# Kernel tuning notes

Hardware: AMD Instinct MI355X
Metric: run time of the kernel (lower is better)

The kernel has to match this reference:

```python
import jax, jax.numpy as jnp
from jax import lax
import numpy as np

NUM_REGIONS = 64
REGION_SIZE = 8
TAU = 13
ETA = 0.8
BINS = 100


def _histc(v, bins=BINS):
    # torch.histc semantics: bins span [min, max]; value==max lands in last bin.
    vmin, vmax = v.min(), v.max()
    idx = jnp.clip(((v - vmin) / (vmax - vmin) * bins), 0, bins - 1).astype(jnp.int32)
    return jnp.bincount(idx, length=bins).astype(jnp.float32)


def setup_inputs() -> dict:
    key = jax.random.key(0)
    x = jax.random.normal(key, (4, 8, 16, 256, 256), dtype=jnp.float32)
    return {"input_tensor": x}


def reference(input_tensor):
    B, T, C, H, W = input_tensor.shape
    rs = REGION_SIZE
    gh, gw = H // rs, W // rs
    G = gh * gw
    nf = T - 1
    R = NUM_REGIONS

    # preprocess: (B,T,C,gh,rs,gw,rs) -> (B,T,C,gh,gw,rs,rs) -> (B,T,C,G,rs,rs)
    fm = input_tensor.reshape(B, T, C, gh, rs, gw, rs)
    fm = fm.transpose(0, 1, 2, 3, 5, 4, 6).reshape(B, T, C, G, rs, rs)

    # motion information (per-batch histogram mutual information)
    motion = fm[:, 1:] - fm[:, :-1]                      # (B,nf,C,G,rs,rs)
    x_t = fm[:, :-1].reshape(B, -1)
    x_t1 = fm[:, 1:].reshape(B, -1)
    n_el = x_t.shape[1]

    h_joint = jax.vmap(_histc)(x_t * x_t1)               # (B,100)
    h_x = jax.vmap(_histc)(x_t) / n_el
    h_x1 = jax.vmap(_histc)(x_t1) / n_el
    p_joint = h_joint / h_joint.sum(-1, keepdims=True)
    p_x = h_x / h_x.sum(-1, keepdims=True)
    p_x1 = h_x1 / h_x1.sum(-1, keepdims=True)
    mi = (p_joint * (jnp.log(p_joint + 1e-10) - jnp.log(p_x * p_x1 + 1e-10))).sum(-1)  # (B,)
    corr = (np.e ** ETA) / jnp.tanh(jnp.log(mi))
    motion = motion + corr[:, None, None, None, None, None]

    # select top regions: sum over channels, topk over G*rs*rs flattened
    mag = motion.reshape(B, nf, C, -1).sum(axis=2)       # (B,nf,G*rs*rs)
    _, top_idx = lax.top_k(mag, R)                       # (B,nf,R)

    # spatial centers (faithful to original: divisor is num_regions)
    y_idx = top_idx // R
    x_idx = top_idx % R
    cy = (y_idx * rs + rs // 2).astype(jnp.float32)
    cx = (x_idx * rs + rs // 2).astype(jnp.float32)
    centers = jnp.stack([cy, cx], axis=-1)               # (B,nf,R,2)

    mean_c = centers.mean(axis=2, keepdims=True)
    d = centers - mean_c
    cov = jnp.einsum('bfri,bfrj->bfij', d, d) / (R - 1)  # (B,nf,2,2)
    inv_cov = jnp.linalg.inv(cov + 1e-6 * jnp.eye(2, dtype=cov.dtype))

    # diff = centers.unsqueeze(2) - centers.unsqueeze(3) -> (B,nf,R,R,2)
    diff = centers[:, :, None, :, :] - centers[:, :, :, None, :]
    v = jnp.einsum('bfqre,bfed->bfqrd', diff, inv_cov)
    maha = jnp.sqrt(v * diff).sum(-1)                    # (B,nf,R,R)

    # graph: mark tau^2 smallest distances with 1
    flat = maha.reshape(B, nf, R * R)
    _, ti = lax.top_k(-flat, TAU * TAU)                  # smallest
    b_ix = jnp.arange(B)[:, None, None]
    f_ix = jnp.arange(nf)[None, :, None]
    graph = jnp.zeros_like(flat).at[b_ix, f_ix, ti].set(1.0)
    return graph.reshape(B, nf, R, R)
```

## Files before the change

kernel.cpp:

```cpp
#include <hip/hip_runtime.h>
#include <stdint.h>


typedef unsigned int u32;
typedef unsigned long long u64;

#define BB 4
#define TT 8
#define CC 16
#define HWN 65536
#define NF 7
#define FRAME 1048576LL
#define NELF 7340032.0f
#define NPAIR 28
#define SEG 65536

#define WS_MM 0
#define WS_CORR 128
#define WS_WCNT 144
#define WS_MAG 16384
#define WS_MMPART (WS_MAG)
#define WS_HISTC  (WS_MAG + 65536)
#define WS_NEED (16384 + 28LL*65536*4)

__device__ __forceinline__ u32 encf(float f) {
  u32 u = __float_as_uint(f);
  return (u & 0x80000000u) ? ~u : (u | 0x80000000u);
}
__device__ __forceinline__ float decf(u32 e) {
  u32 u = (e & 0x80000000u) ? (e ^ 0x80000000u) : ~e;
  return __uint_as_float(u);
}

__global__ void k_minmax_pass(const float* __restrict__ x, u32* __restrict__ part) {
  const int blk = blockIdx.x;
  const int b = blk >> 9;
  const long long w0 = (long long)(blk & 511) * 2048;
  const int tid = threadIdx.x;
  u32 mn0 = 0xFFFFFFFFu, mx0 = 0u, mn1 = 0xFFFFFFFFu, mx1 = 0u,
      mnp = 0xFFFFFFFFu, mxp = 0u;
  float4 pv0, pv1;
  for (int t = 0; t < 8; ++t) {
    const float4* fp = (const float4*)(x + ((long long)(b * TT + t)) * FRAME + w0);
    float4 v0 = fp[tid];
    float4 v1 = fp[tid + 256];
#define MM_COMP(vc, pc)                                                     \
    {                                                                       \
      u32 ev = encf(vc);                                                    \
      if (t < 7) { mn0 = min(mn0, ev); mx0 = max(mx0, ev); }                \
      if (t > 0) {                                                          \
        mn1 = min(mn1, ev); mx1 = max(mx1, ev);                             \
        u32 ep = encf(__fmul_rn(pc, vc));                                   \
        mnp = min(mnp, ep); mxp = max(mxp, ep);                             \
      }                                                                     \
    }
    MM_COMP(v0.x, pv0.x) MM_COMP(v0.y, pv0.y) MM_COMP(v0.z, pv0.z) MM_COMP(v0.w, pv0.w)
    MM_COMP(v1.x, pv1.x) MM_COMP(v1.y, pv1.y) MM_COMP(v1.z, pv1.z) MM_COMP(v1.w, pv1.w)
#undef MM_COMP
    pv0 = v0; pv1 = v1;
  }
  __shared__ u32 sm[6][256];
  sm[0][tid] = mn0; sm[1][tid] = mx0; sm[2][tid] = mn1;
  sm[3][tid] = mx1; sm[4][tid] = mnp; sm[5][tid] = mxp;
  __syncthreads();
  for (int st = 128; st > 0; st >>= 1) {
    if (tid < st) {
      sm[0][tid] = min(sm[0][tid], sm[0][tid + st]);
      sm[1][tid] = max(sm[1][tid], sm[1][tid + st]);
      sm[2][tid] = min(sm[2][tid], sm[2][tid + st]);
      sm[3][tid] = max(sm[3][tid], sm[3][tid + st]);
      sm[4][tid] = min(sm[4][tid], sm[4][tid + st]);
      sm[5][tid] = max(sm[5][tid], sm[5][tid + st]);
    }
    __syncthreads();
  }
  if (tid == 0) {
    u32* o = part + blk * 6;
    o[0] = sm[0][0]; o[1] = sm[1][0]; o[2] = sm[2][0];
    o[3] = sm[3][0]; o[4] = sm[4][0]; o[5] = sm[5][0];
  }
}

__global__ void k_mm_reduce(const u32* __restrict__ part, u32* __restrict__ mm) {
  const int b = blockIdx.x;
  const int tid = threadIdx.x;
  const u32* p0 = part + (b * 512 + tid) * 6;
  const u32* p1 = p0 + 256 * 6;
  __shared__ u32 sm[6][256];
  sm[0][tid] = min(p0[0], p1[0]); sm[1][tid] = max(p0[1], p1[1]);
  sm[2][tid] = min(p0[2], p1[2]); sm[3][tid] = max(p0[3], p1[3]);
  sm[4][tid] = min(p0[4], p1[4]); sm[5][tid] = max(p0[5], p1[5]);
  __syncthreads();
  for (int st = 128; st > 0; st >>= 1) {
    if (tid < st) {
      sm[0][tid] = min(sm[0][tid], sm[0][tid + st]);
      sm[1][tid] = max(sm[1][tid], sm[1][tid + st]);
      sm[2][tid] = min(sm[2][tid], sm[2][tid + st]);
      sm[3][tid] = max(sm[3][tid], sm[3][tid + st]);
      sm[4][tid] = min(sm[4][tid], sm[4][tid + st]);
      sm[5][tid] = max(sm[5][tid], sm[5][tid + st]);
    }
    __syncthreads();
  }
  if (tid == 0)
    for (int i = 0; i < 6; ++i) mm[b * 6 + i] = sm[i][0];
}

__device__ __forceinline__ int bin_of(float v, float vmin, float den) {
  float tt = __fsub_rn(v, vmin);
  float q = __fdiv_rn(tt, den);
  float z = __fmul_rn(q, 100.0f);
  z = fminf(fmaxf(z, 0.0f), 99.0f);
  return (int)z;
}

__global__ void k_hist_pass(const float* __restrict__ x, const u32* __restrict__ mm,
                            u32* __restrict__ histc) {
  __shared__ u32 h[300 * 16];
  for (int i = threadIdx.x; i < 4800; i += 256) h[i] = 0u;
  __syncthreads();
  const int blk = blockIdx.x;
  const int b = blk >> 9;
  const long long w0 = (long long)(blk & 511) * 2048;
  const int tid = threadIdx.x;
  const int sub = tid & 15;
  float mn_t = decf(mm[6 * b + 0]), den_t = __fsub_rn(decf(mm[6 * b + 1]), decf(mm[6 * b + 0]));
  float mn_1 = decf(mm[6 * b + 2]), den_1 = __fsub_rn(decf(mm[6 * b + 3]), decf(mm[6 * b + 2]));
  float mn_p = decf(mm[6 * b + 4]), den_p = __fsub_rn(decf(mm[6 * b + 5]), decf(mm[6 * b + 4]));
  float prev[8];
  for (int t = 0; t < 8; ++t) {
    const float* fp = x + ((long long)(b * TT + t)) * FRAME + w0 + tid;
#pragma unroll
    for (int k = 0; k < 8; ++k) {
      float v = fp[k << 8];
      if (t < 7) atomicAdd(&h[bin_of(v, mn_t, den_t) * 16 + sub], 1u);
      if (t > 0) {
        atomicAdd(&h[(100 + bin_of(v, mn_1, den_1)) * 16 + sub], 1u);
        float p = __fmul_rn(prev[k], v);
        atomicAdd(&h[(200 + bin_of(p, mn_p, den_p)) * 16 + sub], 1u);
      }
      prev[k] = v;
    }
  }
  __syncthreads();
  u32* dst = histc + blk * 300;
  for (int i = threadIdx.x; i < 300; i += 256) {
    u32 s = 0;
#pragma unroll
    for (int c = 0; c < 16; ++c) s += h[i * 16 + c];
    dst[i] = s;
  }
}

__device__ float tanh_emul(float a) {
  const float kClamp = 7.90531110763549805f;
  float xx = fminf(fmaxf(a, -kClamp), kClamp);
  float x2 = __fmul_rn(xx, xx);
  float p = __fmaf_rn(x2, -2.76076847742355e-16f, 2.00018790482477e-13f);
  p = __fmaf_rn(x2, p, -8.60467152213735e-11f);
  p = __fmaf_rn(x2, p, 5.12229709037114e-08f);
  p = __fmaf_rn(x2, p, 1.48572235717979e-05f);
  p = __fmaf_rn(x2, p, 6.37261928875436e-04f);
  p = __fmaf_rn(x2, p, 4.89352455891786e-03f);
  p = __fmul_rn(xx, p);
  float q = __fmaf_rn(x2, 1.19825839466702e-06f, 1.18534705686654e-04f);
  q = __fmaf_rn(x2, q, 2.26843463243900e-03f);
  q = __fmaf_rn(x2, q, 4.89352518554385e-03f);
  float r = __fdiv_rn(p, q);
  if (fabsf(a) < 0.0004f) r = a;
  return r;
}

__global__ void __launch_bounds__(256) k_corr(const u32* __restrict__ histc,
                                              float* __restrict__ corr) {
  const int b = blockIdx.x;
  const int tid = threadIdx.x;
  __shared__ u32 shist[300];
  __shared__ float shx[100], shx1[100], sterm[100];
  __shared__ float ssum[3];
  for (int i = tid; i < 300; i += 256) {
    const u32* src = histc + (long long)(b * 512) * 300 + i;
    u32 s0 = 0, s1 = 0, s2 = 0, s3 = 0, s4 = 0, s5 = 0, s6 = 0, s7 = 0;
    for (int c = 0; c < 512; c += 8) {
      s0 += src[(c + 0) * 300]; s1 += src[(c + 1) * 300];
      s2 += src[(c + 2) * 300]; s3 += src[(c + 3) * 300];
      s4 += src[(c + 4) * 300]; s5 += src[(c + 5) * 300];
      s6 += src[(c + 6) * 300]; s7 += src[(c + 7) * 300];
    }
    shist[i] = ((s0 + s1) + (s2 + s3)) + ((s4 + s5) + (s6 + s7));
  }
  __syncthreads();
  const u32* HX = shist;
  const u32* HX1 = shist + 100;
  const u32* HJ = shist + 200;
  if (tid < 100) {
    shx[tid] = __fdiv_rn((float)HX[tid], NELF);
    shx1[tid] = __fdiv_rn((float)HX1[tid], NELF);
  }
  __syncthreads();
  if (tid == 0) {
    float Sj = 0.0f;
    for (int i = 0; i < 100; ++i) Sj = __fadd_rn(Sj, (float)HJ[i]);
    float Sx = 0.0f, Sx1 = 0.0f;
    for (int i = 0; i < 100; ++i) Sx = __fadd_rn(Sx, shx[i]);
    for (int i = 0; i < 100; ++i) Sx1 = __fadd_rn(Sx1, shx1[i]);
    ssum[0] = Sj; ssum[1] = Sx; ssum[2] = Sx1;
  }
  __syncthreads();
  if (tid < 100) {
    float Sj = ssum[0], Sx = ssum[1], Sx1 = ssum[2];
    float pj = __fdiv_rn((float)HJ[tid], Sj);
    float px = __fdiv_rn(shx[tid], Sx);
    float px1 = __fdiv_rn(shx1[tid], Sx1);
    float la = (float)log((double)__fadd_rn(pj, 1e-10f));
    float lb = (float)log((double)__fadd_rn(__fmul_rn(px, px1), 1e-10f));
    sterm[tid] = __fmul_rn(pj, __fsub_rn(la, lb));
  }
  __syncthreads();
  if (tid == 0) {
    float mi = 0.0f;
    for (int i = 0; i < 100; ++i) mi = __fadd_rn(mi, sterm[i]);
    float lm = (float)log((double)mi);
    float th = tanh_emul(lm);
    float num = (float)exp(0.8);
    corr[b] = __fdiv_rn(num, th);
  }
}

__global__ void k_mag_all(const float* __restrict__ x, const float* __restrict__ corr,
                          float* __restrict__ mag) {
  int gid = blockIdx.x * 256 + threadIdx.x;
  int b = gid >> 16;
  int hw = gid & 65535;
  int row = hw >> 8, col = hw & 255;
  int g = (row >> 3) * 32 + (col >> 3);
  int s = g * 64 + (row & 7) * 8 + (col & 7);
  const float cb = corr[b];
  const float* xp = x + (long long)b * TT * FRAME + hw;
  float acc[7] = {0.f, 0.f, 0.f, 0.f, 0.f, 0.f, 0.f};
  for (int c = 0; c < CC; ++c) {
    float v[8];
#pragma unroll
    for (int t = 0; t < 8; ++t)
      v[t] = xp[(long long)(t * CC + c) << 16];
#pragma unroll
    for (int f = 0; f < 7; ++f)
      acc[f] = __fadd_rn(acc[f], __fadd_rn(__fsub_rn(v[f + 1], v[f]), cb));
  }
#pragma unroll
  for (int f = 0; f < 7; ++f)
    mag[(((long long)(b * NF + f)) << 16) + s] = acc[f];
}

__global__ void __launch_bounds__(64) k_top64_local(const float* __restrict__ mag,
                                                    u64* __restrict__ cand,
                                                    u32* __restrict__ wcnt) {
  const int blk = blockIdx.x;
  const int bf = blk >> 4;
  const int wid = blk & 15;
  const int lane = threadIdx.x;
  const int wbase_elem = wid * 4096;
  const float4* m4 = (const float4*)(mag + (long long)bf * SEG + wbase_elem);

  u32 e[64];
#pragma unroll
  for (int k = 0; k < 16; ++k) {
    float4 v = m4[k * 64 + lane];
    e[4 * k + 0] = encf(v.x); e[4 * k + 1] = encf(v.y);
    e[4 * k + 2] = encf(v.z); e[4 * k + 3] = encf(v.w);
  }
  u32 T = 0u;
  for (int bit = 31; bit >= 0; --bit) {
    u32 Tt = T | (1u << bit);
    u32 c = 0;
#pragma unroll
    for (int k = 0; k < 64; ++k) c += (e[k] >= Tt) ? 1u : 0u;
#pragma unroll
    for (int off = 1; off < 64; off <<= 1) c += __shfl_xor(c, off, 64);
    if (c >= 64u) T = Tt;
  }

  u64* dst = cand + (long long)bf * 2048 + wid * 128;
  u32 run = 0;
  const u64 below = (lane == 0) ? 0ull : (~0ull >> (64 - lane));
#pragma unroll
  for (int k = 0; k < 64; ++k) {
    bool cnd = (e[k] >= T);
    u64 mask = __ballot(cnd);
    if (cnd) {
      u32 off = run + (u32)__popcll(mask & below);
      if (off < 128u) {
        int s = wbase_elem + (k >> 2) * 256 + lane * 4 + (k & 3);
        dst[off] = ((u64)e[k] << 32) | (u64)(0xFFFFFFFFu - (u32)s);
      }
    }
    run += (u32)__popcll(mask);
  }
  if (lane == 0) wcnt[bf * 16 + wid] = (run < 128u) ? run : 128u;
}

__global__ void __launch_bounds__(1024) k_merge_graph(const u64* __restrict__ cand,
                                                      const u32* __restrict__ wcnt,
                                                      float* __restrict__ out) {
  const int bf = blockIdx.x;
  const int tid = threadIdx.x;
  __shared__ u64 candk[2048];
  __shared__ u32 wbase[17];
  __shared__ float cy[64], cx[64];
  __shared__ float sinv[4];
  __shared__ u32 keys[4096];
  __shared__ u32 bins[256 * 16];
  __shared__ u32 stot[256];
  __shared__ u32 tie[4096];
  __shared__ u32 scal[4];

  if (tid == 0) {
    u32 acc = 0;
    for (int w = 0; w < 16; ++w) { wbase[w] = acc; acc += wcnt[bf * 16 + w]; }
    wbase[16] = acc;
  }
  __syncthreads();
  for (int w = 0; w < 16; ++w) {
    u32 cnt = wbase[w + 1] - wbase[w];
    for (u32 s = tid; s < cnt; s += 1024)
      candk[wbase[w] + s] = cand[(long long)bf * 2048 + w * 128 + s];
  }
  __syncthreads();
  u32 n = wbase[16];

  for (u32 i = tid; i < n; i += 1024) {
    u64 mine = candk[i];
    int rank = 0;
    for (u32 j = 0; j < n; ++j) rank += (candk[j] > mine) ? 1 : 0;
    if (rank < 64) {
      int idx = (int)(0xFFFFFFFFu - (u32)(mine & 0xFFFFFFFFull));
      cy[rank] = (float)((idx >> 6) * 8 + 4);
      cx[rank] = (float)((idx & 63) * 8 + 4);
    }
  }
  __syncthreads();

  if (tid == 0) {
    float sy = 0.f, sx = 0.f;
    for (int r = 0; r < 64; ++r) sy = __fadd_rn(sy, cy[r]);
    for (int r = 0; r < 64; ++r) sx = __fadd_rn(sx, cx[r]);
    float my = __fdiv_rn(sy, 64.0f), mx = __fdiv_rn(sx, 64.0f);
    float c00 = 0.f, c01 = 0.f, c11 = 0.f;
    for (int r = 0; r < 64; ++r) {
      float dy = __fsub_rn(cy[r], my);
      float dx = __fsub_rn(cx[r], mx);
      c00 = __fadd_rn(c00, __fmul_rn(dy, dy));
      c01 = __fadd_rn(c01, __fmul_rn(dy, dx));
      c11 = __fadd_rn(c11, __fmul_rn(dx, dx));
    }
    c00 = __fdiv_rn(c00, 63.0f); c01 = __fdiv_rn(c01, 63.0f); c11 = __fdiv_rn(c11, 63.0f);
    c00 = __fadd_rn(c00, 1e-6f); c11 = __fadd_rn(c11, 1e-6f);
    double det = (double)c00 * (double)c11 - (double)c01 * (double)c01;
    sinv[0] = (float)((double)c11 / det);
    sinv[1] = (float)(-(double)c01 / det);
    sinv[2] = sinv[1];
    sinv[3] = (float)((double)c00 / det);
  }
  __syncthreads();

  float i00 = sinv[0], i01 = sinv[1], i10 = sinv[2], i11 = sinv[3];
  long long obase = (long long)bf * 4096;
  for (int ee = tid; ee < 4096; ee += 1024) {
    int q = ee >> 6, r = ee & 63;
    float d0 = __fsub_rn(cy[r], cy[q]);
    float d1 = __fsub_rn(cx[r], cx[q]);
    float v0 = __fadd_rn(__fadd_rn(0.0f, __fmul_rn(d0, i00)), __fmul_rn(d1, i10));
    float v1 = __fadd_rn(__fadd_rn(0.0f, __fmul_rn(d0, i01)), __fmul_rn(d1, i11));
    float p0 = __fmul_rn(v0, d0);
    float p1 = __fmul_rn(v1, d1);
    float s0 = __fsqrt_rn(p0);
    float s1 = __fsqrt_rn(p1);
    float mh = __fadd_rn(__fadd_rn(0.0f, s0), s1);
    u32 key;
    if (mh != mh) key = 0xFFFFFFFFu;
    else key = encf(-mh);
    keys[ee] = key;
    out[obase + ee] = 0.0f;
  }
  __syncthreads();

  u32 prefix = 0u, need = 169u;
  for (int pass = 0; pass < 4; ++pass) {
    int shift = 24 - pass * 8;
    if (tid == 0) scal[2] = 0u;
    for (int i = tid; i < 4096; i += 1024) bins[i] = 0u;
    __syncthreads();
    for (int k = 0; k < 4; ++k) {
      u32 ky = keys[tid + (k << 10)];
      bool ok = (pass == 0) || ((ky >> (shift + 8)) == (prefix >> (shift + 8)));
      if (ok) atomicAdd(&bins[(((ky >> shift) & 0xFFu) << 4) + (tid & 15)], 1u);
    }
    __syncthreads();
    if (tid < 256) {
      u32 s = 0;
#pragma unroll
      for (int c = 0; c < 16; ++c) s += bins[(tid << 4) + c];
      stot[tid] = s;
    }
    __syncthreads();
    for (int off = 1; off < 256; off <<= 1) {
      u32 v = 0;
      if (tid < 256) {
        v = stot[tid];
        if (tid + off < 256) v += stot[tid + off];
      }
      __syncthreads();
      if (tid < 256) stot[tid] = v;
      __syncthreads();
    }
    if (tid < 256) {
      u32 si = stot[tid];
      u32 snext = (tid < 255) ? stot[tid + 1] : 0u;
      if (si >= need && snext < need) {
        scal[0] = prefix | ((u32)tid << shift);
        scal[1] = need - snext;
      }
    }
    __syncthreads();
    prefix = scal[0]; need = scal[1];
    __syncthreads();
  }
  for (int k = 0; k < 4; ++k) {
    int ee = tid + (k << 10);
    u32 ky = keys[ee];
    if (ky > prefix) out[obase + ee] = 1.0f;
    else if (ky == prefix) {
      u32 p = atomicAdd(&scal[2], 1u);
      tie[p] = (u32)ee;
    }
  }
  __syncthreads();
  int tc = (int)scal[2];
  for (int i = tid; i < tc; i += 1024) {
    u32 ei = tie[i];
    int rank = 0;
    for (int j = 0; j < tc; ++j) rank += (tie[j] < ei);
    if (rank < (int)need) out[obase + ei] = 1.0f;
  }
}

extern "C" void kernel_launch(void* const* d_in, const int* in_sizes, int n_in,
                              void* d_out, int out_size, void* d_ws, size_t ws_size,
                              hipStream_t stream) {
  if (ws_size < (size_t)WS_NEED) return;
  const float* x = (const float*)d_in[0];
  float* out = (float*)d_out;
  char* ws = (char*)d_ws;
  u32* mm = (u32*)(ws + WS_MM);
  float* corr = (float*)(ws + WS_CORR);
  u32* wcnt = (u32*)(ws + WS_WCNT);
  float* mag = (float*)(ws + WS_MAG);
  u32* mmpart = (u32*)(ws + WS_MMPART);
  u32* histc = (u32*)(ws + WS_HISTC);
  u64* cand = (u64*)d_out;

  hipLaunchKernelGGL(k_minmax_pass, dim3(2048), dim3(256), 0, stream, x, mmpart);
  hipLaunchKernelGGL(k_mm_reduce, dim3(4), dim3(256), 0, stream, mmpart, mm);
  hipLaunchKernelGGL(k_hist_pass, dim3(2048), dim3(256), 0, stream, x, mm, histc);
  hipLaunchKernelGGL(k_corr, dim3(4), dim3(256), 0, stream, histc, corr);
  hipLaunchKernelGGL(k_mag_all, dim3(1024), dim3(256), 0, stream, x, corr, mag);
  hipLaunchKernelGGL(k_top64_local, dim3(448), dim3(64), 0, stream, mag, cand, wcnt);
  hipLaunchKernelGGL(k_merge_graph, dim3(28), dim3(1024), 0, stream, cand, wcnt, out);
}
```

Baseline: 211.7 us.

## Vectorize hist and mag loads with float4, widen shared histogram privatization

The histogram pass now loads four floats per thread with float4 and uses 32 sub-histograms instead of 16, so the shared-memory atomics contend less. Its reduction reads the copies with a rotated index to avoid bank conflicts. The magnitude kernel processes four pixels per thread with float4 loads and stores, launching a quarter of the blocks. The merge kernel's radix bins are likewise widened to 32 copies, which doubles shared memory use and may reduce occupancy.

```diff
diff --git a/kernel.cpp b/kernel.cpp
--- a/kernel.cpp
+++ b/kernel.cpp
@@ -116,38 +116,43 @@
 
 __global__ void k_hist_pass(const float* __restrict__ x, const u32* __restrict__ mm,
                             u32* __restrict__ histc) {
-  __shared__ u32 h[300 * 16];
-  for (int i = threadIdx.x; i < 4800; i += 256) h[i] = 0u;
+  __shared__ u32 h[300 * 32];
+  for (int i = threadIdx.x; i < 9600; i += 256) h[i] = 0u;
   __syncthreads();
   const int blk = blockIdx.x;
   const int b = blk >> 9;
   const long long w0 = (long long)(blk & 511) * 2048;
   const int tid = threadIdx.x;
-  const int sub = tid & 15;
+  const int sub = tid & 31;
   float mn_t = decf(mm[6 * b + 0]), den_t = __fsub_rn(decf(mm[6 * b + 1]), decf(mm[6 * b + 0]));
   float mn_1 = decf(mm[6 * b + 2]), den_1 = __fsub_rn(decf(mm[6 * b + 3]), decf(mm[6 * b + 2]));
   float mn_p = decf(mm[6 * b + 4]), den_p = __fsub_rn(decf(mm[6 * b + 5]), decf(mm[6 * b + 4]));
-  float prev[8];
+  float4 pv0, pv1;
   for (int t = 0; t < 8; ++t) {
-    const float* fp = x + ((long long)(b * TT + t)) * FRAME + w0 + tid;
-#pragma unroll
-    for (int k = 0; k < 8; ++k) {
-      float v = fp[k << 8];
-      if (t < 7) atomicAdd(&h[bin_of(v, mn_t, den_t) * 16 + sub], 1u);
-      if (t > 0) {
-        atomicAdd(&h[(100 + bin_of(v, mn_1, den_1)) * 16 + sub], 1u);
-        float p = __fmul_rn(prev[k], v);
-        atomicAdd(&h[(200 + bin_of(p, mn_p, den_p)) * 16 + sub], 1u);
-      }
-      prev[k] = v;
-    }
+    const float4* fp = (const float4*)(x + ((long long)(b * TT + t)) * FRAME + w0);
+    float4 v0 = fp[tid];
+    float4 v1 = fp[tid + 256];
+#define HH_COMP(vc, pc)                                                       \
+    {                                                                         \
+      if (t < 7) atomicAdd(&h[bin_of(vc, mn_t, den_t) * 32 + sub], 1u);       \
+      if (t > 0) {                                                            \
+        atomicAdd(&h[(100 + bin_of(vc, mn_1, den_1)) * 32 + sub], 1u);        \
+        float p = __fmul_rn(pc, vc);                                          \
+        atomicAdd(&h[(200 + bin_of(p, mn_p, den_p)) * 32 + sub], 1u);         \
+      }                                                                       \
+    }
+    HH_COMP(v0.x, pv0.x) HH_COMP(v0.y, pv0.y) HH_COMP(v0.z, pv0.z) HH_COMP(v0.w, pv0.w)
+    HH_COMP(v1.x, pv1.x) HH_COMP(v1.y, pv1.y) HH_COMP(v1.z, pv1.z) HH_COMP(v1.w, pv1.w)
+#undef HH_COMP
+    pv0 = v0; pv1 = v1;
   }
   __syncthreads();
   u32* dst = histc + blk * 300;
   for (int i = threadIdx.x; i < 300; i += 256) {
     u32 s = 0;
 #pragma unroll
-    for (int c = 0; c < 16; ++c) s += h[i * 16 + c];
+    for (int c = 0; c < 32; ++c)
+      s += h[i * 32 + ((c + i) & 31)];
     dst[i] = s;
   }
 }
@@ -230,26 +235,33 @@
 __global__ void k_mag_all(const float* __restrict__ x, const float* __restrict__ corr,
                           float* __restrict__ mag) {
   int gid = blockIdx.x * 256 + threadIdx.x;
-  int b = gid >> 16;
-  int hw = gid & 65535;
-  int row = hw >> 8, col = hw & 255;
+  int b = gid >> 14;
+  int hw0 = (gid & 16383) << 2;
+  int row = hw0 >> 8, col = hw0 & 255;
   int g = (row >> 3) * 32 + (col >> 3);
-  int s = g * 64 + (row & 7) * 8 + (col & 7);
+  int s0 = g * 64 + (row & 7) * 8 + (col & 7);
   const float cb = corr[b];
-  const float* xp = x + (long long)b * TT * FRAME + hw;
-  float acc[7] = {0.f, 0.f, 0.f, 0.f, 0.f, 0.f, 0.f};
+  const float4* xp = (const float4*)(x + (long long)b * TT * FRAME + hw0);
+  float4 acc[7];
+#pragma unroll
+  for (int f = 0; f < 7; ++f) acc[f] = make_float4(0.f, 0.f, 0.f, 0.f);
   for (int c = 0; c < CC; ++c) {
-    float v[8];
+    float4 v[8];
 #pragma unroll
     for (int t = 0; t < 8; ++t)
-      v[t] = xp[(long long)(t * CC + c) << 16];
-#pragma unroll
-    for (int f = 0; f < 7; ++f)
-      acc[f] = __fadd_rn(acc[f], __fadd_rn(__fsub_rn(v[f + 1], v[f]), cb));
-  }
+      v[t] = xp[(t * CC + c) << 14];
+#pragma unroll
+    for (int f = 0; f < 7; ++f) {
+      acc[f].x = __fadd_rn(acc[f].x, __fadd_rn(__fsub_rn(v[f + 1].x, v[f].x), cb));
+      acc[f].y = __fadd_rn(acc[f].y, __fadd_rn(__fsub_rn(v[f + 1].y, v[f].y), cb));
+      acc[f].z = __fadd_rn(acc[f].z, __fadd_rn(__fsub_rn(v[f + 1].z, v[f].z), cb));
+      acc[f].w = __fadd_rn(acc[f].w, __fadd_rn(__fsub_rn(v[f + 1].w, v[f].w), cb));
+    }
+  }
+  float4* mp = (float4*)(mag + (((long long)(b * NF)) << 16));
 #pragma unroll
   for (int f = 0; f < 7; ++f)
-    mag[(((long long)(b * NF + f)) << 16) + s] = acc[f];
+    mp[(f << 14) + (s0 >> 2)] = acc[f];
 }
 
 __global__ void __launch_bounds__(64) k_top64_local(const float* __restrict__ mag,
@@ -309,7 +321,7 @@
   __shared__ float cy[64], cx[64];
   __shared__ float sinv[4];
   __shared__ u32 keys[4096];
-  __shared__ u32 bins[256 * 16];
+  __shared__ u32 bins[256 * 32];
   __shared__ u32 stot[256];
   __shared__ u32 tie[4096];
   __shared__ u32 scal[4];
@@ -388,18 +400,18 @@
   for (int pass = 0; pass < 4; ++pass) {
     int shift = 24 - pass * 8;
     if (tid == 0) scal[2] = 0u;
-    for (int i = tid; i < 4096; i += 1024) bins[i] = 0u;
+    for (int i = tid; i < 8192; i += 1024) bins[i] = 0u;
     __syncthreads();
     for (int k = 0; k < 4; ++k) {
       u32 ky = keys[tid + (k << 10)];
       bool ok = (pass == 0) || ((ky >> (shift + 8)) == (prefix >> (shift + 8)));
-      if (ok) atomicAdd(&bins[(((ky >> shift) & 0xFFu) << 4) + (tid & 15)], 1u);
+      if (ok) atomicAdd(&bins[(((ky >> shift) & 0xFFu) << 5) + (tid & 31)], 1u);
     }
     __syncthreads();
     if (tid < 256) {
       u32 s = 0;
 #pragma unroll
-      for (int c = 0; c < 16; ++c) s += bins[(tid << 4) + c];
+      for (int c = 0; c < 32; ++c) s += bins[(tid << 5) + ((c + tid) & 31)];
       stot[tid] = s;
     }
     __syncthreads();
@@ -463,7 +475,7 @@
   hipLaunchKernelGGL(k_mm_reduce, dim3(4), dim3(256), 0, stream, mmpart, mm);
   hipLaunchKernelGGL(k_hist_pass, dim3(2048), dim3(256), 0, stream, x, mm, histc);
   hipLaunchKernelGGL(k_corr, dim3(4), dim3(256), 0, stream, histc, corr);
-  hipLaunchKernelGGL(k_mag_all, dim3(1024), dim3(256), 0, stream, x, corr, mag);
+  hipLaunchKernelGGL(k_mag_all, dim3(256), dim3(256), 0, stream, x, corr, mag);
   hipLaunchKernelGGL(k_top64_local, dim3(448), dim3(64), 0, stream, mag, cand, wcnt);
   hipLaunchKernelGGL(k_merge_graph, dim3(28), dim3(1024), 0, stream, cand, wcnt, out);
 }
```

Result: faster. 205.2 us (-3.1%).
